# Optimization experiments

Hardware: AMD Instinct MI355X
Metric: run time of the kernel (lower is better)

## Reference

```python
import jax, jax.numpy as jnp
import numpy as np

N_NODES = 100000
N_EDGES = 640000
N_LABEL = 100000
IN_C, HID_C, OUT_C = 128, 128, 64


def setup_inputs() -> dict:
    key = jax.random.key(0)
    ks = jax.random.split(key, 9)
    x = jax.random.normal(ks[0], (N_NODES, IN_C), dtype=jnp.float32)
    edge_index = jax.random.randint(ks[1], (2, N_EDGES), 0, N_NODES, dtype=jnp.int64)
    edge_label_index = jax.random.randint(ks[2], (2, N_LABEL), 0, N_NODES, dtype=jnp.int64)
    s = 0.05  # small init scale
    # PyG SAGEConv: lin_l applied to mean-aggregated neighbors (with bias), lin_r to root (no bias)
    W1l = jax.random.normal(ks[3], (HID_C, IN_C), dtype=jnp.float32) * s
    b1 = jnp.zeros((HID_C,), dtype=jnp.float32)
    W1r = jax.random.normal(ks[4], (HID_C, IN_C), dtype=jnp.float32) * s
    W2l = jax.random.normal(ks[5], (OUT_C, HID_C), dtype=jnp.float32) * s
    b2 = jnp.zeros((OUT_C,), dtype=jnp.float32)
    W2r = jax.random.normal(ks[6], (OUT_C, HID_C), dtype=jnp.float32) * s
    return {"x": x, "edge_index": edge_index, "edge_label_index": edge_label_index,
            "W1l": W1l, "b1": b1, "W1r": W1r, "W2l": W2l, "b2": b2, "W2r": W2r}


def _sage_conv(x, src, dst, Wl, b, Wr):
    # mean aggregation of source features at destination nodes
    agg = jax.ops.segment_sum(x[src], dst, num_segments=N_NODES)  # [N, d]
    cnt = jax.ops.segment_sum(jnp.ones((src.shape[0],), x.dtype), dst, num_segments=N_NODES)
    mean = agg / jnp.maximum(cnt, 1.0)[:, None]
    return mean @ Wl.T + b + x @ Wr.T


def reference(x, edge_index, edge_label_index, W1l, b1, W1r, W2l, b2, W2r):
    src, dst = edge_index[0], edge_index[1]
    h = jax.nn.relu(_sage_conv(x, src, dst, W1l, b1, W1r))
    z = _sage_conv(h, src, dst, W2l, b2, W2r)
    # edge-wise dot-product decode
    scores = jnp.sum(z[edge_label_index[0]] * z[edge_label_index[1]], axis=-1)  # [E_label]
    return scores
```

## Files before the change

### kernel.cpp

```cpp
#include <hip/hip_runtime.h>

#define N_NODES 100000
#define N_EDGES 640000
#define N_LABEL 100000
#define CAP 32

typedef __bf16 bf16x8 __attribute__((ext_vector_type(8)));
typedef float f32x4 __attribute__((ext_vector_type(4)));

#define CW1L 0
#define CB1  16384
#define CW1R 16512
#define CW2L 32896
#define CB2  41088
#define CW2R 41152
#define NWTS 49344

__device__ __forceinline__ float bf2f(unsigned short u) {
    union { unsigned int i; float f; } c; c.i = ((unsigned int)u) << 16; return c.f;
}
__device__ __forceinline__ unsigned short f2bf(float f) {
    union { float f; unsigned int i; } c; c.f = f;
    unsigned int lsb = (c.i >> 16) & 1u;
    c.i += 0x7fffu + lsb;
    return (unsigned short)(c.i >> 16);
}

__global__ void k_detect(const unsigned int* __restrict__ xw,
                         const unsigned int* __restrict__ eiw,
                         int* __restrict__ flags) {
    int l = threadIdx.x;
    unsigned int w = xw[l];
    unsigned short lo = (unsigned short)(w & 0xffffu);
    int e = (lo >> 7) & 0xff;
    bool bf_like = (lo == 0) || (e >= 98 && e <= 138);
    unsigned long long m = __ballot(bf_like);
    unsigned int ew = eiw[2 * l + 1];
    unsigned long long mz = __ballot(ew == 0u);
    if (l == 0) {
        flags[0] = (__popcll(m) < 48) ? 1 : 0;
        flags[1] = (__popcll(mz) == 64) ? 1 : 0;
    }
}

__global__ void k_convw(const void* W1l, const void* b1, const void* W1r,
                        const void* W2l, const void* b2, const void* W2r,
                        unsigned short* __restrict__ wts, const int* __restrict__ flags) {
    int i = blockIdx.x * blockDim.x + threadIdx.x;
    if (i >= NWTS) return;
    int f32m = flags[0];
    const void* src; int local;
    if      (i < CB1)  { src = W1l; local = i; }
    else if (i < CW1R) { src = b1;  local = i - CB1; }
    else if (i < CW2L) { src = W1r; local = i - CW1R; }
    else if (i < CB2)  { src = W2l; local = i - CW2L; }
    else if (i < CW2R) { src = b2;  local = i - CB2; }
    else               { src = W2r; local = i - CW2R; }
    wts[i] = f32m ? f2bf(((const float*)src)[local]) : ((const unsigned short*)src)[local];
}

__global__ void k_convx(const void* __restrict__ x, unsigned short* __restrict__ xb,
                        const int* __restrict__ flags) {
    int i = blockIdx.x * blockDim.x + threadIdx.x;
    if (i >= N_NODES * 32) return;
    if (flags[0]) {
        float4 p = ((const float4*)x)[i];
        ushort4 o;
        o.x = f2bf(p.x); o.y = f2bf(p.y); o.z = f2bf(p.z); o.w = f2bf(p.w);
        ((ushort4*)xb)[i] = o;
    } else {
        ((ushort4*)xb)[i] = ((const ushort4*)x)[i];
    }
}

__global__ void k_fill(const int* __restrict__ ei, int* __restrict__ cnt,
                       int* __restrict__ csr, const int* __restrict__ flags) {
    int e = blockIdx.x * blockDim.x + threadIdx.x;
    if (e >= N_EDGES) return;
    int i64 = flags[1];
    int src = ei[e << i64], dst = ei[(N_EDGES + e) << i64];
    int pos = atomicAdd(&cnt[dst], 1);
    if (pos < CAP) csr[dst * CAP + pos] = src;
}

__global__ __launch_bounds__(256) void k_gemm1f(
    const int* __restrict__ cnt, const int* __restrict__ csr,
    const unsigned short* __restrict__ xb, const unsigned short* __restrict__ wts,
    unsigned short* __restrict__ h)
{
    __shared__ unsigned short smean[32][136];
    int wave = threadIdx.x >> 6, lane = threadIdx.x & 63;
    int nb0 = blockIdx.x * 32;

    int nA = nb0 + wave * 8;
    int half = lane >> 5, sl = lane & 31;
    int rows[4];
#pragma unroll
    for (int p = 0; p < 4; ++p)
        rows[p] = csr[(size_t)(nA + p * 2 + half) * CAP + sl];
    int dpre = (lane < 8) ? cnt[nA + lane] : 0;
    int g = lane >> 4, q = lane & 15;
#pragma unroll
    for (int j = 0; j < 8; ++j) {
        int deg = __shfl(dpre, j);
        int m = deg < CAP ? deg : CAP;
        int srcrow = rows[j >> 1];
        int ebase = (j & 1) * 32;
        float s[8];
#pragma unroll
        for (int jj = 0; jj < 8; ++jj) s[jj] = 0.f;
        for (int e0 = 0; e0 < m; e0 += 4) {
            int e = e0 + g;
            int sidx = __shfl(srcrow, ebase + e);
            if (e < m) {
                uint4 w = *(const uint4*)(xb + (size_t)sidx * 128 + q * 8);
                s[0] += bf2f((unsigned short)w.x); s[1] += bf2f((unsigned short)(w.x >> 16));
                s[2] += bf2f((unsigned short)w.y); s[3] += bf2f((unsigned short)(w.y >> 16));
                s[4] += bf2f((unsigned short)w.z); s[5] += bf2f((unsigned short)(w.z >> 16));
                s[6] += bf2f((unsigned short)w.w); s[7] += bf2f((unsigned short)(w.w >> 16));
            }
        }
#pragma unroll
        for (int off = 16; off < 64; off <<= 1)
#pragma unroll
            for (int jj = 0; jj < 8; ++jj) s[jj] += __shfl_xor(s[jj], off);
        if (g == 0) {
            float inv = 1.0f / (deg > 1 ? (float)deg : 1.0f);
            uint4 o;
            o.x = (unsigned int)f2bf(s[0] * inv) | ((unsigned int)f2bf(s[1] * inv) << 16);
            o.y = (unsigned int)f2bf(s[2] * inv) | ((unsigned int)f2bf(s[3] * inv) << 16);
            o.z = (unsigned int)f2bf(s[4] * inv) | ((unsigned int)f2bf(s[5] * inv) << 16);
            o.w = (unsigned int)f2bf(s[6] * inv) | ((unsigned int)f2bf(s[7] * inv) << 16);
            *(uint4*)&smean[wave * 8 + j][q * 8] = o;
        }
    }
    __syncthreads();

    int qq = wave;
    int row = lane & 15, kq = lane >> 4;
    bf16x8 Wf[16];
#pragma unroll
    for (int t = 0; t < 2; ++t)
#pragma unroll
        for (int ks = 0; ks < 8; ++ks) {
            const int k0 = ks * 32;
            const unsigned short* base = wts + (k0 < 128 ? CW1L : CW1R)
                + (size_t)(qq * 32 + t * 16 + row) * 128 + (k0 & 127) + kq * 8;
            Wf[t * 8 + ks] = *reinterpret_cast<const bf16x8*>(base);
        }
    int col = lane & 15, rq = lane >> 4;
    float bias0 = bf2f(wts[CB1 + qq * 32 + col]);
    float bias1 = bf2f(wts[CB1 + qq * 32 + 16 + col]);

#pragma unroll
    for (int i = 0; i < 2; ++i) {
        int n0 = nb0 + i * 16;
        bf16x8 Af[8];
#pragma unroll
        for (int ks = 0; ks < 4; ++ks)
            Af[ks] = *reinterpret_cast<const bf16x8*>(&smean[i * 16 + row][ks * 32 + kq * 8]);
        const unsigned short* rx = xb + (size_t)(n0 + row) * 128 + kq * 8;
#pragma unroll
        for (int ks = 0; ks < 4; ++ks)
            Af[4 + ks] = *reinterpret_cast<const bf16x8*>(rx + ks * 32);
        f32x4 acc0 = (f32x4){0.f, 0.f, 0.f, 0.f};
        f32x4 acc1 = (f32x4){0.f, 0.f, 0.f, 0.f};
#pragma unroll
        for (int ks = 0; ks < 8; ++ks) {
            acc0 = __builtin_amdgcn_mfma_f32_16x16x32_bf16(Af[ks], Wf[ks],     acc0, 0, 0, 0);
            acc1 = __builtin_amdgcn_mfma_f32_16x16x32_bf16(Af[ks], Wf[8 + ks], acc1, 0, 0, 0);
        }
#pragma unroll
        for (int r = 0; r < 4; ++r) {
            int n = n0 + rq * 4 + r;
            float v0 = acc0[r] + bias0; v0 = v0 > 0.f ? v0 : 0.f;
            float v1 = acc1[r] + bias1; v1 = v1 > 0.f ? v1 : 0.f;
            h[(size_t)n * 128 + qq * 32 + col]      = f2bf(v0);
            h[(size_t)n * 128 + qq * 32 + 16 + col] = f2bf(v1);
        }
    }
}

__global__ __launch_bounds__(256) void k_gemm2(
    const unsigned short* __restrict__ h, const unsigned short* __restrict__ wts,
    unsigned short* __restrict__ tb)
{
    int w = (int)((blockIdx.x * blockDim.x + threadIdx.x) >> 6);
    int lane = threadIdx.x & 63;
    int q = w & 3;
    int tg = w >> 2;
    int row = lane & 15, kq = lane >> 4;

    const size_t wbase = (q < 2) ? (CW2L + (size_t)(q * 32) * 128)
                                 : (CW2R + (size_t)((q - 2) * 32) * 128);
    bf16x8 Wf[8];
#pragma unroll
    for (int t = 0; t < 2; ++t)
#pragma unroll
        for (int ks = 0; ks < 4; ++ks)
            Wf[t * 4 + ks] = *reinterpret_cast<const bf16x8*>(
                wts + wbase + (size_t)(t * 16 + row) * 128 + ks * 32 + kq * 8);

    int col = lane & 15, rq = lane >> 4;
    int nt0 = tg * 2;
    bf16x8 Af[2][4];

#define LOAD_A2(tile, buf)                                                            \
    {                                                                                 \
        int n0_ = (tile) * 16;                                                        \
        if (n0_ < N_NODES) {                                                          \
            const unsigned short* rh = h + (size_t)(n0_ + row) * 128 + kq * 8;        \
            _Pragma("unroll")                                                         \
            for (int ks = 0; ks < 4; ++ks)                                            \
                Af[buf][ks] = *reinterpret_cast<const bf16x8*>(rh + ks * 32);         \
        }                                                                             \
    }

    LOAD_A2(nt0, 0);
#pragma unroll
    for (int i = 0; i < 2; ++i) {
        int n0 = (nt0 + i) * 16;
        if (n0 >= N_NODES) continue;
        if (i < 1) LOAD_A2(nt0 + i + 1, (i + 1) & 1);
        f32x4 acc0 = (f32x4){0.f, 0.f, 0.f, 0.f};
        f32x4 acc1 = (f32x4){0.f, 0.f, 0.f, 0.f};
#pragma unroll
        for (int ks = 0; ks < 4; ++ks) {
            acc0 = __builtin_amdgcn_mfma_f32_16x16x32_bf16(Af[i & 1][ks], Wf[ks],     acc0, 0, 0, 0);
            acc1 = __builtin_amdgcn_mfma_f32_16x16x32_bf16(Af[i & 1][ks], Wf[4 + ks], acc1, 0, 0, 0);
        }
#pragma unroll
        for (int r = 0; r < 4; ++r) {
            int n = n0 + rq * 4 + r;
            tb[(size_t)n * 128 + q * 32 + col]      = f2bf(acc0[r]);
            tb[(size_t)n * 128 + q * 32 + 16 + col] = f2bf(acc1[r]);
        }
    }
#undef LOAD_A2
}

__global__ __launch_bounds__(256) void k_agg2c(
    const int* __restrict__ cnt, const int* __restrict__ csr,
    const unsigned short* __restrict__ tb, const unsigned short* __restrict__ wts,
    float* __restrict__ z) {
    int n = (int)((blockIdx.x * blockDim.x + threadIdx.x) >> 6);
    if (n >= N_NODES) return;
    int lane = threadIdx.x & 63;
    int g = lane >> 3, q = lane & 7;
    int deg = cnt[n];
    int m = deg < CAP ? deg : CAP;
    int srcl = (lane < m) ? csr[(size_t)n * CAP + lane] : 0;
    float s[8];
#pragma unroll
    for (int j = 0; j < 8; ++j) s[j] = 0.f;
    for (int e0 = 0; e0 < m; e0 += 8) {
        int e = e0 + g;
        int sidx = __shfl(srcl, e);
        if (e < m) {
            uint4 w = *(const uint4*)(tb + (size_t)sidx * 128 + q * 8);
            s[0] += bf2f((unsigned short)w.x); s[1] += bf2f((unsigned short)(w.x >> 16));
            s[2] += bf2f((unsigned short)w.y); s[3] += bf2f((unsigned short)(w.y >> 16));
            s[4] += bf2f((unsigned short)w.z); s[5] += bf2f((unsigned short)(w.z >> 16));
            s[6] += bf2f((unsigned short)w.w); s[7] += bf2f((unsigned short)(w.w >> 16));
        }
    }
#pragma unroll
    for (int off = 8; off < 64; off <<= 1)
#pragma unroll
        for (int j = 0; j < 8; ++j) s[j] += __shfl_xor(s[j], off);
    if (g == 0) {
        float inv = 1.0f / (deg > 1 ? (float)deg : 1.0f);
        uint4 tr = *(const uint4*)(tb + (size_t)n * 128 + 64 + q * 8);
        uint4 bb = *(const uint4*)(wts + CB2 + q * 8);
        float4 z0, z1;
        z0.x = s[0] * inv + bf2f((unsigned short)bb.x)         + bf2f((unsigned short)tr.x);
        z0.y = s[1] * inv + bf2f((unsigned short)(bb.x >> 16)) + bf2f((unsigned short)(tr.x >> 16));
        z0.z = s[2] * inv + bf2f((unsigned short)bb.y)         + bf2f((unsigned short)tr.y);
        z0.w = s[3] * inv + bf2f((unsigned short)(bb.y >> 16)) + bf2f((unsigned short)(tr.y >> 16));
        z1.x = s[4] * inv + bf2f((unsigned short)bb.z)         + bf2f((unsigned short)tr.z);
        z1.y = s[5] * inv + bf2f((unsigned short)(bb.z >> 16)) + bf2f((unsigned short)(tr.z >> 16));
        z1.z = s[6] * inv + bf2f((unsigned short)bb.w)         + bf2f((unsigned short)tr.w);
        z1.w = s[7] * inv + bf2f((unsigned short)(bb.w >> 16)) + bf2f((unsigned short)(tr.w >> 16));
        *(float4*)(z + (size_t)n * 64 + q * 8)     = z0;
        *(float4*)(z + (size_t)n * 64 + q * 8 + 4) = z1;
    }
}

__global__ void k_decode(const int* __restrict__ eli, const float* __restrict__ z,
                         void* __restrict__ out, const int* __restrict__ flags) {
    long long t = (long long)blockIdx.x * blockDim.x + threadIdx.x;
    int e = (int)(t >> 4);
    if (e >= N_LABEL) return;
    int f32m = flags[0], i64 = flags[1];
    int q = threadIdx.x & 15;
    int a = eli[e << i64], b = eli[(N_LABEL + e) << i64];
    float4 pa = *(const float4*)(z + (size_t)a * 64 + q * 4);
    float4 pb = *(const float4*)(z + (size_t)b * 64 + q * 4);
    float s = pa.x * pb.x + pa.y * pb.y + pa.z * pb.z + pa.w * pb.w;
#pragma unroll
    for (int off = 1; off < 16; off <<= 1) s += __shfl_xor(s, off);
    if (q == 0) {
        if (f32m) ((float*)out)[e] = s;
        else      ((unsigned short*)out)[e] = f2bf(s);
    }
}

extern "C" void kernel_launch(void* const* d_in, const int* in_sizes, int n_in,
                              void* d_out, int out_size, void* d_ws, size_t ws_size,
                              hipStream_t stream) {
    const void* x   = d_in[0];
    const int*  ei  = (const int*)d_in[1];
    const int*  eli = (const int*)d_in[2];
    const void* W1l = d_in[3];
    const void* b1  = d_in[4];
    const void* W1r = d_in[5];
    const void* W2l = d_in[6];
    const void* b2  = d_in[7];
    const void* W2r = d_in[8];

    char* ws = (char*)d_ws;
    const size_t offFlag = 0;
    const size_t offCnt  = 1024;
    const size_t offWts  = 801024;
    const size_t offCsr  = 1u << 20;
    const size_t offXb   = offCsr + (size_t)N_NODES * CAP * 4;
    const size_t offTb   = offXb  + (size_t)N_NODES * 128 * 2;
    const size_t offHz   = offTb  + (size_t)N_NODES * 128 * 2;

    int*            flags = (int*)(ws + offFlag);
    int*            cnt   = (int*)(ws + offCnt);
    unsigned short* wts   = (unsigned short*)(ws + offWts);
    int*            csr   = (int*)(ws + offCsr);
    unsigned short* xb    = (unsigned short*)(ws + offXb);
    unsigned short* tb    = (unsigned short*)(ws + offTb);
    unsigned short* h     = (unsigned short*)(ws + offHz);

    hipMemsetAsync(ws, 0, 1u << 20, stream);

    k_detect<<<1, 64, 0, stream>>>((const unsigned int*)x, (const unsigned int*)ei, flags);
    k_convw<<<(NWTS + 255) / 256, 256, 0, stream>>>(W1l, b1, W1r, W2l, b2, W2r, wts, flags);
    k_convx<<<(N_NODES * 32 + 255) / 256, 256, 0, stream>>>(x, xb, flags);
    k_fill<<<(N_EDGES + 255) / 256, 256, 0, stream>>>(ei, cnt, csr, flags);

    k_gemm1f<<<N_NODES / 32, 256, 0, stream>>>(cnt, csr, xb, wts, h);

    k_gemm2<<<3125, 256, 0, stream>>>(h, wts, tb);

    float* z = (float*)(ws + offHz);
    {
        long long thr = (long long)N_NODES * 64;
        k_agg2c<<<(unsigned)((thr + 255) / 256), 256, 0, stream>>>(cnt, csr, tb, wts, z);
    }

    {
        long long thr = (long long)N_LABEL * 16;
        k_decode<<<(unsigned)((thr + 255) / 256), 256, 0, stream>>>(eli, z, d_out, flags);
    }
}
```

Baseline: 279.5 us.

## Restructure neighbor gathers to per-lane column slices with 8-way batched loads

The two aggregation kernels now give each lane a 2-element column slice and let it walk all neighbors itself, issuing 8 independent 4-byte gathers per iteration. This replaces the old split of neighbors across lane groups, which needed a cross-lane shuffle reduction at the end. The layer-2 aggregation also packs two nodes into each wave, and the weight and feature conversion kernels are merged into one launch. The trade-off is narrower 4-byte loads instead of 16-byte ones, and lanes in a wave now diverge when the two packed nodes have different degrees.

```diff
diff --git a/kernel.cpp b/kernel.cpp
--- a/kernel.cpp
+++ b/kernel.cpp
@@ -15,6 +15,9 @@
 #define CB2  41088
 #define CW2R 41152
 #define NWTS 49344
+
+#define NB_W 193
+#define NB_X 12500
 
 __device__ __forceinline__ float bf2f(unsigned short u) {
     union { unsigned int i; float f; } c; c.i = ((unsigned int)u) << 16; return c.f;
@@ -43,33 +46,35 @@
     }
 }
 
-__global__ void k_convw(const void* W1l, const void* b1, const void* W1r,
-                        const void* W2l, const void* b2, const void* W2r,
-                        unsigned short* __restrict__ wts, const int* __restrict__ flags) {
-    int i = blockIdx.x * blockDim.x + threadIdx.x;
-    if (i >= NWTS) return;
+__global__ void k_convwx(const void* W1l, const void* b1, const void* W1r,
+                         const void* W2l, const void* b2, const void* W2r,
+                         unsigned short* __restrict__ wts,
+                         const void* __restrict__ x, unsigned short* __restrict__ xb,
+                         const int* __restrict__ flags) {
+    int b = blockIdx.x;
     int f32m = flags[0];
-    const void* src; int local;
-    if      (i < CB1)  { src = W1l; local = i; }
-    else if (i < CW1R) { src = b1;  local = i - CB1; }
-    else if (i < CW2L) { src = W1r; local = i - CW1R; }
-    else if (i < CB2)  { src = W2l; local = i - CW2L; }
-    else if (i < CW2R) { src = b2;  local = i - CB2; }
-    else               { src = W2r; local = i - CW2R; }
-    wts[i] = f32m ? f2bf(((const float*)src)[local]) : ((const unsigned short*)src)[local];
-}
-
-__global__ void k_convx(const void* __restrict__ x, unsigned short* __restrict__ xb,
-                        const int* __restrict__ flags) {
-    int i = blockIdx.x * blockDim.x + threadIdx.x;
-    if (i >= N_NODES * 32) return;
-    if (flags[0]) {
-        float4 p = ((const float4*)x)[i];
-        ushort4 o;
-        o.x = f2bf(p.x); o.y = f2bf(p.y); o.z = f2bf(p.z); o.w = f2bf(p.w);
-        ((ushort4*)xb)[i] = o;
+    if (b < NB_W) {
+        int i = b * 256 + threadIdx.x;
+        if (i >= NWTS) return;
+        const void* src; int local;
+        if      (i < CB1)  { src = W1l; local = i; }
+        else if (i < CW1R) { src = b1;  local = i - CB1; }
+        else if (i < CW2L) { src = W1r; local = i - CW1R; }
+        else if (i < CB2)  { src = W2l; local = i - CW2L; }
+        else if (i < CW2R) { src = b2;  local = i - CB2; }
+        else               { src = W2r; local = i - CW2R; }
+        wts[i] = f32m ? f2bf(((const float*)src)[local]) : ((const unsigned short*)src)[local];
     } else {
-        ((ushort4*)xb)[i] = ((const ushort4*)x)[i];
+        int i = (b - NB_W) * 256 + threadIdx.x;
+        if (i >= N_NODES * 32) return;
+        if (f32m) {
+            float4 p = ((const float4*)x)[i];
+            ushort4 o;
+            o.x = f2bf(p.x); o.y = f2bf(p.y); o.z = f2bf(p.z); o.w = f2bf(p.w);
+            ((ushort4*)xb)[i] = o;
+        } else {
+            ((ushort4*)xb)[i] = ((const ushort4*)x)[i];
+        }
     }
 }
 
@@ -99,40 +104,32 @@
     for (int p = 0; p < 4; ++p)
         rows[p] = csr[(size_t)(nA + p * 2 + half) * CAP + sl];
     int dpre = (lane < 8) ? cnt[nA + lane] : 0;
-    int g = lane >> 4, q = lane & 15;
+    int c2 = lane << 1;
+
 #pragma unroll
     for (int j = 0; j < 8; ++j) {
         int deg = __shfl(dpre, j);
         int m = deg < CAP ? deg : CAP;
-        int srcrow = rows[j >> 1];
-        int ebase = (j & 1) * 32;
-        float s[8];
-#pragma unroll
-        for (int jj = 0; jj < 8; ++jj) s[jj] = 0.f;
-        for (int e0 = 0; e0 < m; e0 += 4) {
-            int e = e0 + g;
-            int sidx = __shfl(srcrow, ebase + e);
-            if (e < m) {
-                uint4 w = *(const uint4*)(xb + (size_t)sidx * 128 + q * 8);
-                s[0] += bf2f((unsigned short)w.x); s[1] += bf2f((unsigned short)(w.x >> 16));
-                s[2] += bf2f((unsigned short)w.y); s[3] += bf2f((unsigned short)(w.y >> 16));
-                s[4] += bf2f((unsigned short)w.z); s[5] += bf2f((unsigned short)(w.z >> 16));
-                s[6] += bf2f((unsigned short)w.w); s[7] += bf2f((unsigned short)(w.w >> 16));
+        float s0 = 0.f, s1 = 0.f;
+        for (int e0 = 0; e0 < m; e0 += 8) {
+            unsigned int v[8];
+#pragma unroll
+            for (int u = 0; u < 8; ++u) {
+                int e = e0 + u;
+                int sidx = __shfl(rows[j >> 1], (j & 1) * 32 + e);
+                sidx = (e < m) ? sidx : 0;
+                v[u] = *(const unsigned int*)(xb + (size_t)sidx * 128 + c2);
             }
-        }
-#pragma unroll
-        for (int off = 16; off < 64; off <<= 1)
-#pragma unroll
-            for (int jj = 0; jj < 8; ++jj) s[jj] += __shfl_xor(s[jj], off);
-        if (g == 0) {
-            float inv = 1.0f / (deg > 1 ? (float)deg : 1.0f);
-            uint4 o;
-            o.x = (unsigned int)f2bf(s[0] * inv) | ((unsigned int)f2bf(s[1] * inv) << 16);
-            o.y = (unsigned int)f2bf(s[2] * inv) | ((unsigned int)f2bf(s[3] * inv) << 16);
-            o.z = (unsigned int)f2bf(s[4] * inv) | ((unsigned int)f2bf(s[5] * inv) << 16);
-            o.w = (unsigned int)f2bf(s[6] * inv) | ((unsigned int)f2bf(s[7] * inv) << 16);
-            *(uint4*)&smean[wave * 8 + j][q * 8] = o;
-        }
+#pragma unroll
+            for (int u = 0; u < 8; ++u) {
+                bool ok = (e0 + u) < m;
+                s0 += ok ? bf2f((unsigned short)(v[u] & 0xffffu)) : 0.f;
+                s1 += ok ? bf2f((unsigned short)(v[u] >> 16)) : 0.f;
+            }
+        }
+        float inv = 1.0f / (deg > 1 ? (float)deg : 1.0f);
+        unsigned int o = (unsigned int)f2bf(s0 * inv) | ((unsigned int)f2bf(s1 * inv) << 16);
+        *(unsigned int*)&smean[wave * 8 + j][c2] = o;
     }
     __syncthreads();
 
@@ -243,47 +240,43 @@
     const int* __restrict__ cnt, const int* __restrict__ csr,
     const unsigned short* __restrict__ tb, const unsigned short* __restrict__ wts,
     float* __restrict__ z) {
-    int n = (int)((blockIdx.x * blockDim.x + threadIdx.x) >> 6);
-    if (n >= N_NODES) return;
+    int wv = (int)((blockIdx.x * blockDim.x + threadIdx.x) >> 6);
+    int n2 = wv * 2;
+    if (n2 >= N_NODES) return;
     int lane = threadIdx.x & 63;
-    int g = lane >> 3, q = lane & 7;
-    int deg = cnt[n];
+    int half = lane >> 5, sl = lane & 31;
+    int n = n2 + half;
+    int dpre = (lane < 2) ? cnt[n2 + lane] : 0;
+    int deg = __shfl(dpre, half);
     int m = deg < CAP ? deg : CAP;
-    int srcl = (lane < m) ? csr[(size_t)n * CAP + lane] : 0;
-    float s[8];
-#pragma unroll
-    for (int j = 0; j < 8; ++j) s[j] = 0.f;
-    for (int e0 = 0; e0 < m; e0 += 8) {
-        int e = e0 + g;
-        int sidx = __shfl(srcl, e);
-        if (e < m) {
-            uint4 w = *(const uint4*)(tb + (size_t)sidx * 128 + q * 8);
-            s[0] += bf2f((unsigned short)w.x); s[1] += bf2f((unsigned short)(w.x >> 16));
-            s[2] += bf2f((unsigned short)w.y); s[3] += bf2f((unsigned short)(w.y >> 16));
-            s[4] += bf2f((unsigned short)w.z); s[5] += bf2f((unsigned short)(w.z >> 16));
-            s[6] += bf2f((unsigned short)w.w); s[7] += bf2f((unsigned short)(w.w >> 16));
-        }
-    }
-#pragma unroll
-    for (int off = 8; off < 64; off <<= 1)
-#pragma unroll
-        for (int j = 0; j < 8; ++j) s[j] += __shfl_xor(s[j], off);
-    if (g == 0) {
-        float inv = 1.0f / (deg > 1 ? (float)deg : 1.0f);
-        uint4 tr = *(const uint4*)(tb + (size_t)n * 128 + 64 + q * 8);
-        uint4 bb = *(const uint4*)(wts + CB2 + q * 8);
-        float4 z0, z1;
-        z0.x = s[0] * inv + bf2f((unsigned short)bb.x)         + bf2f((unsigned short)tr.x);
-        z0.y = s[1] * inv + bf2f((unsigned short)(bb.x >> 16)) + bf2f((unsigned short)(tr.x >> 16));
-        z0.z = s[2] * inv + bf2f((unsigned short)bb.y)         + bf2f((unsigned short)tr.y);
-        z0.w = s[3] * inv + bf2f((unsigned short)(bb.y >> 16)) + bf2f((unsigned short)(tr.y >> 16));
-        z1.x = s[4] * inv + bf2f((unsigned short)bb.z)         + bf2f((unsigned short)tr.z);
-        z1.y = s[5] * inv + bf2f((unsigned short)(bb.z >> 16)) + bf2f((unsigned short)(tr.z >> 16));
-        z1.z = s[6] * inv + bf2f((unsigned short)bb.w)         + bf2f((unsigned short)tr.w);
-        z1.w = s[7] * inv + bf2f((unsigned short)(bb.w >> 16)) + bf2f((unsigned short)(tr.w >> 16));
-        *(float4*)(z + (size_t)n * 64 + q * 8)     = z0;
-        *(float4*)(z + (size_t)n * 64 + q * 8 + 4) = z1;
-    }
+    int mo = __shfl(m, lane ^ 32);
+    int mmax = m > mo ? m : mo;
+    int srcrow = csr[(size_t)n * CAP + sl];
+    int c2 = sl << 1;
+    float s0 = 0.f, s1 = 0.f;
+    for (int e0 = 0; e0 < mmax; e0 += 8) {
+        unsigned int v[8];
+#pragma unroll
+        for (int u = 0; u < 8; ++u) {
+            int e = e0 + u;
+            int sidx = __shfl(srcrow, half * 32 + e);
+            sidx = (e < m) ? sidx : 0;
+            v[u] = *(const unsigned int*)(tb + (size_t)sidx * 128 + c2);
+        }
+#pragma unroll
+        for (int u = 0; u < 8; ++u) {
+            bool ok = (e0 + u) < m;
+            s0 += ok ? bf2f((unsigned short)(v[u] & 0xffffu)) : 0.f;
+            s1 += ok ? bf2f((unsigned short)(v[u] >> 16)) : 0.f;
+        }
+    }
+    float inv = 1.0f / (deg > 1 ? (float)deg : 1.0f);
+    unsigned int tr = *(const unsigned int*)(tb + (size_t)n * 128 + 64 + c2);
+    unsigned int bb = *(const unsigned int*)(wts + CB2 + c2);
+    float2 o;
+    o.x = s0 * inv + bf2f((unsigned short)(bb & 0xffffu)) + bf2f((unsigned short)(tr & 0xffffu));
+    o.y = s1 * inv + bf2f((unsigned short)(bb >> 16))     + bf2f((unsigned short)(tr >> 16));
+    *(float2*)(z + (size_t)n * 64 + c2) = o;
 }
 
 __global__ void k_decode(const int* __restrict__ eli, const float* __restrict__ z,
@@ -338,8 +331,9 @@
     hipMemsetAsync(ws, 0, 1u << 20, stream);
 
     k_detect<<<1, 64, 0, stream>>>((const unsigned int*)x, (const unsigned int*)ei, flags);
-    k_convw<<<(NWTS + 255) / 256, 256, 0, stream>>>(W1l, b1, W1r, W2l, b2, W2r, wts, flags);
-    k_convx<<<(N_NODES * 32 + 255) / 256, 256, 0, stream>>>(x, xb, flags);
+
+    k_convwx<<<NB_W + NB_X, 256, 0, stream>>>(W1l, b1, W1r, W2l, b2, W2r, wts, x, xb, flags);
+
     k_fill<<<(N_EDGES + 255) / 256, 256, 0, stream>>>(ei, cnt, csr, flags);
 
     k_gemm1f<<<N_NODES / 32, 256, 0, stream>>>(cnt, csr, xb, wts, h);
@@ -347,10 +341,7 @@
     k_gemm2<<<3125, 256, 0, stream>>>(h, wts, tb);
 
     float* z = (float*)(ws + offHz);
-    {
-        long long thr = (long long)N_NODES * 64;
-        k_agg2c<<<(unsigned)((thr + 255) / 256), 256, 0, stream>>>(cnt, csr, tb, wts, z);
-    }
+    k_agg2c<<<12500, 256, 0, stream>>>(cnt, csr, tb, wts, z);
 
     {
         long long thr = (long long)N_LABEL * 16;
```

After: 259.3 us. 1.08x faster.
